# Performance work log

Measured on AMD Instinct MI355X. Metric: run time of the kernel, lower is better.

## Reference

```python
import jax, jax.numpy as jnp
import numpy as np

K_F = 3
NUM = K_F * K_F - 1      # 8 non-reference neighbors
IDX_REF = NUM // 2       # 4
PROP_TIME = 6
PAD = (K_F - 1) // 2


def _bilinear(img, ys, xs):
    """img: [B,H,W]; ys, xs: [B,K,H,W] float sample positions.
    Bilinear interpolation with zero padding (per-corner validity), matching
    mmcv modulated deformable conv sampling."""
    B, H, W = img.shape
    y0 = jnp.floor(ys); x0 = jnp.floor(xs)
    wy = ys - y0; wx = xs - x0
    y0i = y0.astype(jnp.int32); x0i = x0.astype(jnp.int32)
    b = jnp.arange(B).reshape(B, 1, 1, 1)

    def g(yi, xi):
        valid = (yi >= 0) & (yi < H) & (xi >= 0) & (xi < W)
        v = img[b, jnp.clip(yi, 0, H - 1), jnp.clip(xi, 0, W - 1)]
        return jnp.where(valid, v, 0.0)

    return (g(y0i, x0i) * (1 - wy) * (1 - wx)
            + g(y0i, x0i + 1) * (1 - wy) * wx
            + g(y0i + 1, x0i) * wy * (1 - wx)
            + g(y0i + 1, x0i + 1) * wy * wx)


def setup_inputs() -> dict:
    key = jax.random.key(0)
    ks = jax.random.split(key, 6)
    B, Cg, H, W = 4, 64, 240, 1216
    return {
        "feat_init": jax.random.normal(ks[0], (B, 1, H, W), jnp.float32),
        "guidance": jax.random.normal(ks[1], (B, Cg, H, W), jnp.float32),
        "confidence": jax.random.uniform(ks[2], (B, 1, H, W), dtype=jnp.float32),
        "feat_fix": jax.random.normal(ks[3], (B, 1, H, W), jnp.float32),
        "conv_w": jax.random.normal(ks[4], (3 * NUM, Cg, 3, 3), jnp.float32) * 0.05,
        "conv_b": jax.random.normal(ks[5], (3 * NUM,), jnp.float32) * 0.01,
        "aff_scale_const": jnp.full((1,), 0.5 * NUM, jnp.float32),  # affinity_gamma * num (TGASS)
    }


def reference(feat_init, guidance, confidence, feat_fix, conv_w, conv_b, aff_scale_const):
    B, _, H, W = guidance.shape
    dt = guidance.dtype
    sg = jax.lax.stop_gradient

    # offset/affinity head: [B, 3*num, H, W]
    oa = jax.lax.conv_general_dilated(
        guidance, conv_w, (1, 1), ((PAD, PAD), (PAD, PAD)),
        dimension_numbers=("NCHW", "OIHW", "NCHW")) + conv_b[None, :, None, None]
    o1, o2, aff = oa[:, :NUM], oa[:, NUM:2 * NUM], oa[:, 2 * NUM:]

    # insert zero offset at reference position -> [B, 9, H, W] each
    zero = jnp.zeros((B, 1, H, W), dt)
    dy = jnp.concatenate([o1[:, :IDX_REF], zero, o1[:, IDX_REF:]], axis=1)
    dx = jnp.concatenate([o2[:, :IDX_REF], zero, o2[:, IDX_REF:]], axis=1)

    # TGASS affinity
    aff = jnp.tanh(aff) / (aff_scale_const[0] + 1e-8)

    # confidence propagation: 1x1 deform conv (w_conf=1, b=0, pad=0) per
    # non-center kernel point, offsets detached -> bilinear sample of confidence
    idx_nc = jnp.array([0, 1, 2, 3, 5, 6, 7, 8])
    hgrid = jnp.arange(H, dtype=dt)[:, None]
    wgrid = jnp.arange(W, dtype=dt)
    conf_aff = _bilinear(confidence[:, 0],
                         sg(dy[:, idx_nc]) + hgrid,
                         sg(dx[:, idx_nc]) + wgrid)  # [B,8,H,W]
    aff = aff * conf_aff

    # normalize (ASS/TGASS clamp sum to >= 1)
    s = jnp.maximum(jnp.sum(jnp.abs(aff), axis=1, keepdims=True) + 1e-4, 1.0)
    aff = aff / s
    aff_ref = 1.0 - jnp.sum(aff, axis=1, keepdims=True)
    aff9 = jnp.concatenate([aff[:, :IDX_REF], aff_ref, aff[:, IDX_REF:]], axis=1)  # [B,9,H,W]

    # 3x3 deformable sampling grid (pad=1, dilation=1, weight=1, bias=0)
    k = jnp.arange(K_F * K_F)
    base_dy = (k // K_F - PAD).astype(dt)[None, :, None, None]
    base_dx = (k % K_F - PAD).astype(dt)[None, :, None, None]
    ys = hgrid + base_dy + dy  # [B,9,H,W]
    xs = wgrid + base_dx + dx

    mask_fix = sg((feat_fix > 0.0).astype(dt))
    feat = feat_init
    for _ in range(PROP_TIME):
        feat = (1.0 - mask_fix) * feat + mask_fix * feat_fix
        feat = jnp.sum(aff9 * _bilinear(feat[:, 0], ys, xs), axis=1, keepdims=True)

    offset_flat = jnp.stack([dy, dx], axis=2).reshape(B, 2 * (NUM + 1), H, W)
    return feat, offset_flat, aff9
```

## Files before the change

### kernel.cpp

```cpp
#include <hip/hip_runtime.h>
#include <hip/hip_bf16.h>
#include <math.h>

#define B_ 4
#define CG_ 64
#define H_ 240
#define W_ 1216
#define NUMK 576
#define WP (W_ + 2)
#define HP (H_ + 2)
#define WPAD (W_ + 4)
#define HPAD (H_ + 4)
#define PPLANE ((size_t)HPAD * WPAD)

#define TCC 32
#define THR 8
#define SRr 10
#define SCc 34
#define NWT2 (W_ / TCC)
#define NHT2 (H_ / THR)
#define NBLK3 (NWT2 * NHT2 * B_)
#define CBS2 260
#define SMEM_BYTES (SRr * SCc * 128)
#define NCHK (SRr * SCc * 8)

#define R5TC 16
#define R5TH 4
#define R5SC 20
#define R5SR 6
#define R5CPAD 72
#define R5NWT (W_ / R5TC)
#define R5NHT (H_ / R5TH)
#define R5NBLK (R5NWT * R5NHT * B_)
#define R5CBS 68

typedef __attribute__((ext_vector_type(8))) short bf16x8;
typedef __attribute__((ext_vector_type(4))) float f32x4;

__device__ __forceinline__ float bilin_zero(const float* __restrict__ img, float y, float x) {
    float y0f = floorf(y), x0f = floorf(x);
    float wy = y - y0f, wx = x - x0f;
    int y0 = (int)y0f, x0 = (int)x0f;
    int y1 = y0 + 1, x1 = x0 + 1;
    bool yv0 = ((unsigned)y0 < (unsigned)H_);
    bool yv1 = ((unsigned)y1 < (unsigned)H_);
    bool xv0 = ((unsigned)x0 < (unsigned)W_);
    bool xv1 = ((unsigned)x1 < (unsigned)W_);
    float v00 = (yv0 && xv0) ? img[y0 * W_ + x0] : 0.f;
    float v01 = (yv0 && xv1) ? img[y0 * W_ + x1] : 0.f;
    float v10 = (yv1 && xv0) ? img[y1 * W_ + x0] : 0.f;
    float v11 = (yv1 && xv1) ? img[y1 * W_ + x1] : 0.f;
    return v00 * (1.f - wy) * (1.f - wx) + v01 * (1.f - wy) * wx
         + v10 * wy * (1.f - wx) + v11 * wy * wx;
}

__device__ __forceinline__ float bilin_pad(const float* __restrict__ imgp, float y, float x) {
    float yc = fminf(fmaxf(y, -2.0f), (float)H_);
    float xc = fminf(fmaxf(x, -2.0f), (float)W_);
    float y0f = floorf(yc), x0f = floorf(xc);
    float wy = yc - y0f, wx = xc - x0f;
    int iy = (int)y0f + 2, ix = (int)x0f + 2;
    const float* p = imgp + iy * WPAD + ix;
    float v00 = p[0], v01 = p[1], v10 = p[WPAD], v11 = p[WPAD + 1];
    return v00 * (1.f - wy) * (1.f - wx) + v01 * (1.f - wy) * wx
         + v10 * wy * (1.f - wx) + v11 * wy * wx;
}

__device__ __forceinline__ void prep_epilogue(
    const float* a24, int b, int h, int w,
    const float* __restrict__ confidence, const float* __restrict__ feat_init,
    const float* __restrict__ feat_fix, float scale,
    float* __restrict__ out_offset, float* __restrict__ out_aff9,
    float* __restrict__ fb0, unsigned* __restrict__ offb, ushort* __restrict__ affb)
{
    const float* confb = confidence + (size_t)b * H_ * W_;
    float dyv[8], dxv[8], av[8];
    float ssum = 0.f;
    #pragma unroll
    for (int j = 0; j < 8; j++) {
        float dy = a24[j];
        float dx = a24[8 + j];
        float a = tanhf(a24[16 + j]) / scale;
        float conf = bilin_zero(confb, (float)h + dy, (float)w + dx);
        a *= conf;
        dyv[j] = dy; dxv[j] = dx; av[j] = a;
        ssum += fabsf(a);
    }
    float s = fmaxf(ssum + 1e-4f, 1.0f);
    float inv_s = 1.0f / s;
    float suma = 0.f;
    #pragma unroll
    for (int j = 0; j < 8; j++) { av[j] *= inv_s; suma += av[j]; }
    const float aref = 1.0f - suma;

    const int hw = h * W_ + w;
    #pragma unroll
    for (int k = 0; k < 9; k++) {
        float dy = (k == 4) ? 0.f : dyv[(k < 4) ? k : k - 1];
        float dx = (k == 4) ? 0.f : dxv[(k < 4) ? k : k - 1];
        float a  = (k == 4) ? aref : av[(k < 4) ? k : k - 1];
        out_offset[((size_t)(b * 18 + 2 * k) * H_) * W_ + hw] = dy;
        out_offset[((size_t)(b * 18 + 2 * k + 1) * H_) * W_ + hw] = dx;
        out_aff9[((size_t)(b * 9 + k) * H_) * W_ + hw] = a;
        if (offb) {
            __hip_bfloat16 hy = __float2bfloat16(dy);
            __hip_bfloat16 hx = __float2bfloat16(dx);
            __hip_bfloat16 ha = __float2bfloat16(a);
            unsigned uy = *(ushort*)&hy, ux = *(ushort*)&hx;
            offb[((size_t)(b * 9 + k) * H_) * W_ + hw] = uy | (ux << 16);
            affb[((size_t)(b * 9 + k) * H_) * W_ + hw] = *(ushort*)&ha;
        }
    }
    const size_t pix = (size_t)b * H_ * W_ + hw;
    float ff = feat_fix[pix];
    float fi = feat_init[pix];
    float m = (ff > 0.f) ? 1.f : 0.f;
    fb0[pix] = (1.f - m) * fi + m * ff;
}

__global__ __launch_bounds__(256) void zero_pad_kernel(float4* __restrict__ p, int n4) {
    int i = blockIdx.x * 256 + threadIdx.x;
    if (i < n4) p[i] = make_float4(0.f, 0.f, 0.f, 0.f);
}

__global__ __launch_bounds__(256) void pad_conf_kernel(
    const float* __restrict__ confidence, float* __restrict__ confp)
{
    int i = blockIdx.x * 256 + threadIdx.x;
    const int n = B_ * HPAD * WPAD;
    if (i >= n) return;
    int col = i % WPAD;
    int row = (i / WPAD) % HPAD;
    int b = i / (WPAD * HPAD);
    int gh = row - 2, gw = col - 2;
    float v = 0.f;
    if ((unsigned)gh < (unsigned)H_ && (unsigned)gw < (unsigned)W_)
        v = confidence[((size_t)b * H_ + gh) * W_ + gw];
    confp[i] = v;
}

__global__ __launch_bounds__(256) void repack_w_kernel(
    const float* __restrict__ conv_w, __hip_bfloat16* __restrict__ wfrag)
{
    int i = blockIdx.x * 256 + threadIdx.x;
    if (i >= 32 * NUMK) return;
    int e = i & 7;
    int p = (i >> 3) & 15;
    int g = (i >> 7) & 3;
    int half = (i >> 9) & 1;
    int s = i >> 10;
    int m = half * 16 + p;
    int kp = s * 32 + g * 8 + e;
    int tap = kp / 64, c = kp % 64;
    float v = (m < 24) ? conv_w[m * NUMK + c * 9 + tap] : 0.f;
    wfrag[i] = __float2bfloat16(v);
}

__global__ __launch_bounds__(256) void transpose_kernel(
    const float* __restrict__ guidance, __hip_bfloat16* __restrict__ gbf)
{
    __shared__ __align__(16) __hip_bfloat16 tl[64 * 72];
    const int tid = threadIdx.x;
    const int w0 = blockIdx.x * 64;
    const int row = blockIdx.y;
    const int b = blockIdx.z;
    const int gh = row - 1;
    __hip_bfloat16* gbfb = gbf + (size_t)b * HP * WP * 64;

    const int px = tid >> 2;
    const int ch0 = (tid & 3) * 16;
    bf16x8 z8 = {};

    if ((unsigned)gh < (unsigned)H_) {
        const int col = tid & 63;
        const int chb = tid >> 6;
        #pragma unroll
        for (int r = 0; r < 16; r++) {
            int ch = r * 4 + chb;
            float v = guidance[(((size_t)b * CG_ + ch) * H_ + gh) * W_ + w0 + col];
            tl[col * 72 + ch] = __float2bfloat16(v);
        }
        __syncthreads();
        __hip_bfloat16* dst = gbfb + ((size_t)row * WP + 1 + w0 + px) * 64 + ch0;
        *(bf16x8*)dst = *(const bf16x8*)&tl[px * 72 + ch0];
        *(bf16x8*)(dst + 8) = *(const bf16x8*)&tl[px * 72 + ch0 + 8];
    } else {
        __hip_bfloat16* dst = gbfb + ((size_t)row * WP + 1 + w0 + px) * 64 + ch0;
        *(bf16x8*)dst = z8;
        *(bf16x8*)(dst + 8) = z8;
    }
    if (blockIdx.x == 0 && tid < 8)
        *(bf16x8*)(gbfb + ((size_t)row * WP) * 64 + tid * 8) = z8;
    if (blockIdx.x == 18 && tid < 8)
        *(bf16x8*)(gbfb + ((size_t)row * WP + WP - 1) * 64 + tid * 8) = z8;
}

__global__ __launch_bounds__(512, 6) void conv_lds_kernel(
    const __hip_bfloat16* __restrict__ gbf, const __hip_bfloat16* __restrict__ wfrag,
    const float* __restrict__ conv_b, const float* __restrict__ confp,
    const float* __restrict__ feat_init, const float* __restrict__ feat_fix,
    const float* __restrict__ aff_scale,
    float* __restrict__ out_offset, float* __restrict__ out_aff9,
    float* __restrict__ fbp0, unsigned* __restrict__ offb, ushort* __restrict__ affb)
{
    __shared__ __align__(16) char smem[SMEM_BYTES];

    const int tid = threadIdx.x;
    int lin = (blockIdx.x & 7) * (NBLK3 / 8) + (blockIdx.x >> 3);
    const int r0 = lin % NHT2;
    const int rest = lin / NHT2;
    const int wt = rest % NWT2;
    const int b  = rest / NWT2;
    const int h0 = r0 * THR;
    const int w0 = wt * TCC;

    {
        const __hip_bfloat16* gsrc = gbf + (size_t)b * HP * WP * 64;
        auto stage_one = [&](int i) {
            int r = i / (SCc * 8);
            int t = i % (SCc * 8);
            int col = t >> 3;
            int chb = t & 7;
            bf16x8 v = *(const bf16x8*)(gsrc + ((size_t)(h0 + r) * WP + w0 + col) * 64 + chb * 8);
            int dst = (r * SCc + col) * 128 + ((chb * 16) ^ ((col & 7) << 4));
            *(bf16x8*)(smem + dst) = v;
        };
        #pragma unroll
        for (int it = 0; it < 5; it++)
            stage_one(tid + it * 512);
        if (tid < NCHK - 5 * 512)
            stage_one(tid + 5 * 512);
    }
    __syncthreads();

    const int lane = tid & 63;
    const int wid  = tid >> 6;
    const int p    = lane & 15;
    const int g    = lane >> 4;

    f32x4 acc[2][2] = {};

    #pragma unroll
    for (int s = 0; s < 18; s++) {
        const int tap = s >> 1;
        const int ky = tap / 3, kx = tap % 3;
        const int c0b = (s & 1) * 64;
        const __hip_bfloat16* wp = wfrag + (size_t)s * 1024 + g * 128 + p * 8;
        bf16x8 a0 = *(const bf16x8*)(wp);
        bf16x8 a1 = *(const bf16x8*)(wp + 512);
        const int srow = wid + ky;
        #pragma unroll
        for (int nf = 0; nf < 2; nf++) {
            int scol = nf * 16 + p + kx;
            int off = (srow * SCc + scol) * 128 + ((c0b + g * 16) ^ ((scol & 7) << 4));
            bf16x8 bv = *(const bf16x8*)(smem + off);
            acc[0][nf] = __builtin_amdgcn_mfma_f32_16x16x32_bf16(a0, bv, acc[0][nf], 0, 0, 0);
            acc[1][nf] = __builtin_amdgcn_mfma_f32_16x16x32_bf16(a1, bv, acc[1][nf], 0, 0, 0);
        }
    }
    __syncthreads();

    float* cbuf = (float*)smem;
    #pragma unroll
    for (int mt = 0; mt < 2; mt++) {
        int ch = mt * 16 + g * 4;
        if (ch < 24) {
            #pragma unroll
            for (int nf = 0; nf < 2; nf++) {
                int px = wid * 32 + nf * 16 + p;
                #pragma unroll
                for (int r = 0; r < 4; r++)
                    cbuf[(size_t)(ch + r) * CBS2 + px] = acc[mt][nf][r];
            }
        }
    }
    __syncthreads();

    {
        const int pxid = tid >> 1;
        const int sub = tid & 1;
        const int h = h0 + (pxid >> 5);
        const int w = w0 + (pxid & 31);
        const float scale = aff_scale[0] + 1e-8f;
        const float* confb = confp + (size_t)b * PPLANE;

        float dyv[4], dxv[4], av[4];
        float part = 0.f;
        #pragma unroll
        for (int jj = 0; jj < 4; jj++) {
            int j = sub * 4 + jj;
            float dy = cbuf[(size_t)j * CBS2 + pxid] + conv_b[j];
            float dx = cbuf[(size_t)(8 + j) * CBS2 + pxid] + conv_b[8 + j];
            float a = tanhf(cbuf[(size_t)(16 + j) * CBS2 + pxid] + conv_b[16 + j]) / scale;
            float conf = bilin_pad(confb, (float)h + dy, (float)w + dx);
            a *= conf;
            dyv[jj] = dy; dxv[jj] = dx; av[jj] = a;
            part += fabsf(a);
        }
        float ssum = part + __shfl_xor(part, 1);
        float s = fmaxf(ssum + 1e-4f, 1.0f);
        float inv_s = 1.0f / s;
        float sp = 0.f;
        #pragma unroll
        for (int jj = 0; jj < 4; jj++) { av[jj] *= inv_s; sp += av[jj]; }
        float suma = sp + __shfl_xor(sp, 1);

        const int hw = h * W_ + w;
        auto store_k = [&](int k, float dy, float dx, float a) {
            out_offset[((size_t)(b * 18 + 2 * k) * H_) * W_ + hw] = dy;
            out_offset[((size_t)(b * 18 + 2 * k + 1) * H_) * W_ + hw] = dx;
            out_aff9[((size_t)(b * 9 + k) * H_) * W_ + hw] = a;
            __hip_bfloat16 hy = __float2bfloat16(dy);
            __hip_bfloat16 hx = __float2bfloat16(dx);
            __hip_bfloat16 ha = __float2bfloat16(a);
            unsigned uy = *(ushort*)&hy, ux = *(ushort*)&hx;
            offb[((size_t)(b * 9 + k) * H_) * W_ + hw] = uy | (ux << 16);
            affb[((size_t)(b * 9 + k) * H_) * W_ + hw] = *(ushort*)&ha;
        };
        if (sub == 0) {
            #pragma unroll
            for (int jj = 0; jj < 4; jj++)
                store_k(jj, dyv[jj], dxv[jj], av[jj]);
            store_k(4, 0.f, 0.f, 1.0f - suma);
            const size_t pix = (size_t)b * H_ * W_ + hw;
            float ff = feat_fix[pix];
            float fi = feat_init[pix];
            float m = (ff > 0.f) ? 1.f : 0.f;
            fbp0[(size_t)b * PPLANE + (size_t)(h + 2) * WPAD + (w + 2)] =
                (1.f - m) * fi + m * ff;
        } else {
            #pragma unroll
            for (int jj = 0; jj < 4; jj++)
                store_k(5 + jj, dyv[jj], dxv[jj], av[jj]);
        }
    }
}

__global__ __launch_bounds__(256) void prop_packed_kernel(
    const float* __restrict__ fbp_in, const unsigned* __restrict__ offb,
    const ushort* __restrict__ affb, const float* __restrict__ feat_fix,
    float* __restrict__ out, int do_blend, int out_padded)
{
    const int tpx = blockIdx.x * 256 + threadIdx.x;
    const int n2 = (B_ * H_ * W_) / 2;
    if (tpx >= n2) return;
    const int idx = tpx * 2;
    const int w = idx % W_;
    const int h = (idx / W_) % H_;
    const int b = idx / (W_ * H_);
    const float* fbb = fbp_in + (size_t)b * PPLANE;
    const int hw = h * W_ + w;

    float sum0 = 0.f, sum1 = 0.f;
    #pragma unroll
    for (int k = 0; k < 9; k++) {
        const size_t pb = ((size_t)(b * 9 + k) * H_) * W_ + hw;
        uint2 uo = *(const uint2*)(offb + pb);
        unsigned ua = *(const unsigned*)(affb + pb);
        float yb = (float)h + (float)(k / 3 - 1);
        float xb = (float)w + (float)(k % 3 - 1);
        float dy0 = __uint_as_float(uo.x << 16);
        float dx0 = __uint_as_float(uo.x & 0xFFFF0000u);
        float a0  = __uint_as_float(ua << 16);
        sum0 += a0 * bilin_pad(fbb, yb + dy0, xb + dx0);
        float dy1 = __uint_as_float(uo.y << 16);
        float dx1 = __uint_as_float(uo.y & 0xFFFF0000u);
        float a1  = __uint_as_float(ua & 0xFFFF0000u);
        sum1 += a1 * bilin_pad(fbb, yb + dy1, xb + 1.0f + dx1);
    }
    if (do_blend) {
        float2 ff = *(const float2*)(feat_fix + idx);
        if (ff.x > 0.f) sum0 = ff.x;
        if (ff.y > 0.f) sum1 = ff.y;
    }
    if (out_padded) {
        float* o = out + (size_t)b * PPLANE + (size_t)(h + 2) * WPAD + (w + 2);
        *(float2*)o = make_float2(sum0, sum1);
    } else {
        *(float2*)(out + idx) = make_float2(sum0, sum1);
    }
}

__global__ __launch_bounds__(256, 8) void conv_mfma_r5(
    const float* __restrict__ guidance, const __hip_bfloat16* __restrict__ wfrag,
    const float* __restrict__ conv_b, const float* __restrict__ confidence,
    const float* __restrict__ feat_init, const float* __restrict__ feat_fix,
    const float* __restrict__ aff_scale,
    float* __restrict__ out_offset, float* __restrict__ out_aff9,
    float* __restrict__ fb0)
{
    __shared__ __align__(16) __hip_bfloat16 gl[R5SR * R5SC * R5CPAD];
    const int tid = threadIdx.x;
    int lin = (blockIdx.x & 7) * (R5NBLK / 8) + (blockIdx.x >> 3);
    const int r0 = lin % R5NHT;
    const int rest = lin / R5NHT;
    const int wt = rest % R5NWT;
    const int b  = rest / R5NWT;
    const int h0 = r0 * R5TH;
    const int w0 = wt * R5TC;
    {
        auto stage_one = [&](int i) {
            int col = i % R5SC;
            int rest2 = i / R5SC;
            int kr = rest2 % R5SR;
            int c4 = rest2 / R5SR;
            int gh = h0 - 1 + kr;
            int gw = w0 - 2 + col;
            bool vok = ((unsigned)gh < (unsigned)H_) & ((unsigned)gw < (unsigned)W_);
            union { unsigned long long u; __hip_bfloat16 hv[4]; } pk;
            const float* src = guidance + (((size_t)b * CG_ + c4 * 4) * H_ + gh) * W_ + gw;
            #pragma unroll
            for (int j = 0; j < 4; j++) {
                float v = vok ? src[(size_t)j * H_ * W_] : 0.f;
                pk.hv[j] = __float2bfloat16(v);
            }
            *(unsigned long long*)&gl[(size_t)(kr * R5SC + col) * R5CPAD + c4 * 4] = pk.u;
        };
        #pragma unroll
        for (int it = 0; it < 7; it++) stage_one(tid + it * 256);
        if (tid < R5SR * R5SC * 16 - 7 * 256) stage_one(tid + 7 * 256);
    }
    __syncthreads();
    const int lane = tid & 63;
    const int wid  = tid >> 6;
    const int p    = lane & 15;
    const int g    = lane >> 4;
    f32x4 acc[2] = {};
    #pragma unroll
    for (int s = 0; s < 18; s++) {
        const int tap = s >> 1;
        const int ky = tap / 3, kx = tap % 3;
        const int c0 = (s & 1) * 32;
        const __hip_bfloat16* wp = wfrag + (size_t)s * 1024 + g * 128 + p * 8;
        bf16x8 a0 = *(const bf16x8*)(wp);
        bf16x8 a1 = *(const bf16x8*)(wp + 512);
        int cb = p + kx + 1;
        bf16x8 b0 = *(const bf16x8*)(gl + (size_t)((wid + ky) * R5SC + cb) * R5CPAD + c0 + g * 8);
        acc[0] = __builtin_amdgcn_mfma_f32_16x16x32_bf16(a0, b0, acc[0], 0, 0, 0);
        acc[1] = __builtin_amdgcn_mfma_f32_16x16x32_bf16(a1, b0, acc[1], 0, 0, 0);
    }
    __syncthreads();
    float* cbuf = (float*)gl;
    #pragma unroll
    for (int mt = 0; mt < 2; mt++) {
        int ch = mt * 16 + g * 4;
        if (ch < 24) {
            int px = wid * 16 + p;
            #pragma unroll
            for (int r = 0; r < 4; r++)
                cbuf[(size_t)(ch + r) * R5CBS + px] = acc[mt][r];
        }
    }
    __syncthreads();
    if (tid < R5TH * R5TC) {
        const int h = h0 + (tid >> 4);
        const int w = w0 + (tid & 15);
        float a24[24];
        #pragma unroll
        for (int ch = 0; ch < 24; ch++)
            a24[ch] = cbuf[(size_t)ch * R5CBS + tid] + conv_b[ch];
        prep_epilogue(a24, b, h, w, confidence, feat_init, feat_fix,
                      aff_scale[0] + 1e-8f, out_offset, out_aff9, fb0,
                      (unsigned*)nullptr, (ushort*)nullptr);
    }
}

__global__ __launch_bounds__(256) void prop_f32_kernel(
    const float* __restrict__ fb_in, const float* __restrict__ offset,
    const float* __restrict__ aff9, const float* __restrict__ feat_fix,
    float* __restrict__ out, int do_blend)
{
    const int idx = blockIdx.x * 256 + threadIdx.x;
    const int n = B_ * H_ * W_;
    if (idx >= n) return;
    const int w = idx % W_;
    const int h = (idx / W_) % H_;
    const int b = idx / (W_ * H_);
    const float* fbb = fb_in + (size_t)b * H_ * W_;
    const int hw = h * W_ + w;
    float sum = 0.f;
    #pragma unroll
    for (int k = 0; k < 9; k++) {
        float dy = offset[((size_t)(b * 18 + 2 * k) * H_) * W_ + hw];
        float dx = offset[((size_t)(b * 18 + 2 * k + 1) * H_) * W_ + hw];
        float a  = aff9[((size_t)(b * 9 + k) * H_) * W_ + hw];
        float y = (float)h + (float)(k / 3 - 1) + dy;
        float x = (float)w + (float)(k % 3 - 1) + dx;
        sum += a * bilin_zero(fbb, y, x);
    }
    if (do_blend) {
        float ff = feat_fix[idx];
        float m = (ff > 0.f) ? 1.f : 0.f;
        sum = (1.f - m) * sum + m * ff;
    }
    out[idx] = sum;
}

extern "C" void kernel_launch(void* const* d_in, const int* in_sizes, int n_in,
                              void* d_out, int out_size, void* d_ws, size_t ws_size,
                              hipStream_t stream) {
    const float* feat_init  = (const float*)d_in[0];
    const float* guidance   = (const float*)d_in[1];
    const float* confidence = (const float*)d_in[2];
    const float* feat_fix   = (const float*)d_in[3];
    const float* conv_w     = (const float*)d_in[4];
    const float* conv_b     = (const float*)d_in[5];
    const float* aff_scale  = (const float*)d_in[6];

    float* out_feat = (float*)d_out;
    const size_t P1 = (size_t)B_ * H_ * W_;
    float* out_offset = out_feat + P1;
    float* out_aff9   = out_offset + 18 * P1;

    char* ws = (char*)d_ws;
    float* fb0 = (float*)ws;                                   ws += P1 * 4;
    float* fb1 = (float*)ws;                                   ws += P1 * 4;
    __hip_bfloat16* wfrag = (__hip_bfloat16*)ws;               ws += 32 * NUMK * 2;
    unsigned* offb = (unsigned*)ws;                            ws += 9 * P1 * 4;
    ushort* affb = (ushort*)ws;                                ws += 9 * P1 * 2;
    __hip_bfloat16* gbf = (__hip_bfloat16*)ws;                 ws += (size_t)B_ * HP * WP * 64 * 2;
    float* fbp0 = (float*)ws;                                  ws += B_ * PPLANE * 4;
    float* fbp1 = (float*)ws;                                  ws += B_ * PPLANE * 4;
    float* confp = (float*)ws;                                 ws += B_ * PPLANE * 4;
    const size_t need = (size_t)(ws - (char*)d_ws);

    repack_w_kernel<<<(32 * NUMK + 255) / 256, 256, 0, stream>>>(conv_w, wfrag);

    const int n = (int)P1;

    if (ws_size >= need) {
        const int n4 = (int)(2 * B_ * PPLANE / 4);
        zero_pad_kernel<<<(n4 + 255) / 256, 256, 0, stream>>>((float4*)fbp0, n4);
        const int nc = B_ * HPAD * WPAD;
        pad_conf_kernel<<<(nc + 255) / 256, 256, 0, stream>>>(confidence, confp);
        transpose_kernel<<<dim3(19, HP, B_), 256, 0, stream>>>(guidance, gbf);
        conv_lds_kernel<<<NBLK3, 512, 0, stream>>>(
            gbf, wfrag, conv_b, confp, feat_init, feat_fix, aff_scale,
            out_offset, out_aff9, fbp0, offb, affb);
        const int p2blocks = (n / 2 + 255) / 256;
        float* pbufs[2] = {fbp0, fbp1};
        for (int it = 0; it < 6; it++) {
            const float* in = pbufs[it & 1];
            float* o = (it == 5) ? out_feat : pbufs[(it + 1) & 1];
            prop_packed_kernel<<<p2blocks, 256, 0, stream>>>(
                in, offb, affb, feat_fix, o, (it < 5) ? 1 : 0, (it < 5) ? 1 : 0);
        }
    } else {
        const int pblocks = (n + 255) / 256;
        float* bufs[2] = {fb0, fb1};
        conv_mfma_r5<<<R5NBLK, 256, 0, stream>>>(
            guidance, wfrag, conv_b, confidence, feat_init, feat_fix, aff_scale,
            out_offset, out_aff9, fb0);
        for (int it = 0; it < 6; it++) {
            const float* in = bufs[it & 1];
            float* o = (it == 5) ? out_feat : bufs[(it + 1) & 1];
            prop_f32_kernel<<<pblocks, 256, 0, stream>>>(
                in, out_offset, out_aff9, feat_fix, o, (it < 5) ? 1 : 0);
        }
    }
}
```

Baseline: 395.6 us.

## Halve conv tile height and merge zero-pad and confidence-pad kernels

The conv kernel tile shrinks from 8 to 4 output rows per block. Each warp now computes one 16-pixel column fragment instead of two, and four threads share each pixel in the epilogue, with an extra shuffle level for the sums. LDS use drops and launch bounds rise to 8 blocks per SM, aiming at more occupancy and more blocks. The cost is more halo re-staging per output pixel, since 6 staged rows now serve 4 output rows where 10 served 8. The separate zero-fill and confidence-pad kernels are fused into one launch over the three contiguous padded buffers, saving a launch.

```diff
diff --git a/kernel.cpp b/kernel.cpp
--- a/kernel.cpp
+++ b/kernel.cpp
@@ -14,13 +14,13 @@
 #define PPLANE ((size_t)HPAD * WPAD)
 
 #define TCC 32
-#define THR 8
-#define SRr 10
+#define THR 4
+#define SRr 6
 #define SCc 34
 #define NWT2 (W_ / TCC)
 #define NHT2 (H_ / THR)
 #define NBLK3 (NWT2 * NHT2 * B_)
-#define CBS2 260
+#define CBS2 132
 #define SMEM_BYTES (SRr * SCc * 128)
 #define NCHK (SRr * SCc * 8)
 
@@ -118,25 +118,24 @@
     fb0[pix] = (1.f - m) * fi + m * ff;
 }
 
-__global__ __launch_bounds__(256) void zero_pad_kernel(float4* __restrict__ p, int n4) {
+__global__ __launch_bounds__(256) void init_pads_kernel(
+    const float* __restrict__ confidence, float* __restrict__ base)
+{
+    const int n = (int)(3 * B_ * PPLANE);
     int i = blockIdx.x * 256 + threadIdx.x;
-    if (i < n4) p[i] = make_float4(0.f, 0.f, 0.f, 0.f);
-}
-
-__global__ __launch_bounds__(256) void pad_conf_kernel(
-    const float* __restrict__ confidence, float* __restrict__ confp)
-{
-    int i = blockIdx.x * 256 + threadIdx.x;
-    const int n = B_ * HPAD * WPAD;
     if (i >= n) return;
-    int col = i % WPAD;
-    int row = (i / WPAD) % HPAD;
-    int b = i / (WPAD * HPAD);
-    int gh = row - 2, gw = col - 2;
     float v = 0.f;
-    if ((unsigned)gh < (unsigned)H_ && (unsigned)gw < (unsigned)W_)
-        v = confidence[((size_t)b * H_ + gh) * W_ + gw];
-    confp[i] = v;
+    const int cbase = (int)(2 * B_ * PPLANE);
+    if (i >= cbase) {
+        int local = i - cbase;
+        int col = local % WPAD;
+        int row = (local / WPAD) % HPAD;
+        int b = local / (int)PPLANE;
+        int gh = row - 2, gw = col - 2;
+        if ((unsigned)gh < (unsigned)H_ && (unsigned)gw < (unsigned)W_)
+            v = confidence[((size_t)b * H_ + gh) * W_ + gw];
+    }
+    base[i] = v;
 }
 
 __global__ __launch_bounds__(256) void repack_w_kernel(
@@ -195,7 +194,7 @@
         *(bf16x8*)(gbfb + ((size_t)row * WP + WP - 1) * 64 + tid * 8) = z8;
 }
 
-__global__ __launch_bounds__(512, 6) void conv_lds_kernel(
+__global__ __launch_bounds__(512, 8) void conv_lds_kernel(
     const __hip_bfloat16* __restrict__ gbf, const __hip_bfloat16* __restrict__ wfrag,
     const float* __restrict__ conv_b, const float* __restrict__ confp,
     const float* __restrict__ feat_init, const float* __restrict__ feat_fix,
@@ -226,19 +225,21 @@
             *(bf16x8*)(smem + dst) = v;
         };
         #pragma unroll
-        for (int it = 0; it < 5; it++)
+        for (int it = 0; it < 3; it++)
             stage_one(tid + it * 512);
-        if (tid < NCHK - 5 * 512)
-            stage_one(tid + 5 * 512);
+        if (tid < NCHK - 3 * 512)
+            stage_one(tid + 3 * 512);
     }
     __syncthreads();
 
     const int lane = tid & 63;
     const int wid  = tid >> 6;
+    const int wrow = wid >> 1;
+    const int ch16 = (wid & 1) * 16;
     const int p    = lane & 15;
     const int g    = lane >> 4;
 
-    f32x4 acc[2][2] = {};
+    f32x4 acc[2] = {};
 
     #pragma unroll
     for (int s = 0; s < 18; s++) {
@@ -248,15 +249,12 @@
         const __hip_bfloat16* wp = wfrag + (size_t)s * 1024 + g * 128 + p * 8;
         bf16x8 a0 = *(const bf16x8*)(wp);
         bf16x8 a1 = *(const bf16x8*)(wp + 512);
-        const int srow = wid + ky;
-        #pragma unroll
-        for (int nf = 0; nf < 2; nf++) {
-            int scol = nf * 16 + p + kx;
-            int off = (srow * SCc + scol) * 128 + ((c0b + g * 16) ^ ((scol & 7) << 4));
-            bf16x8 bv = *(const bf16x8*)(smem + off);
-            acc[0][nf] = __builtin_amdgcn_mfma_f32_16x16x32_bf16(a0, bv, acc[0][nf], 0, 0, 0);
-            acc[1][nf] = __builtin_amdgcn_mfma_f32_16x16x32_bf16(a1, bv, acc[1][nf], 0, 0, 0);
-        }
+        const int srow = wrow + ky;
+        const int scol = ch16 + p + kx;
+        int off = (srow * SCc + scol) * 128 + ((c0b + g * 16) ^ ((scol & 7) << 4));
+        bf16x8 bv = *(const bf16x8*)(smem + off);
+        acc[0] = __builtin_amdgcn_mfma_f32_16x16x32_bf16(a0, bv, acc[0], 0, 0, 0);
+        acc[1] = __builtin_amdgcn_mfma_f32_16x16x32_bf16(a1, bv, acc[1], 0, 0, 0);
     }
     __syncthreads();
 
@@ -265,30 +263,27 @@
     for (int mt = 0; mt < 2; mt++) {
         int ch = mt * 16 + g * 4;
         if (ch < 24) {
+            int px = wrow * 32 + ch16 + p;
             #pragma unroll
-            for (int nf = 0; nf < 2; nf++) {
-                int px = wid * 32 + nf * 16 + p;
-                #pragma unroll
-                for (int r = 0; r < 4; r++)
-                    cbuf[(size_t)(ch + r) * CBS2 + px] = acc[mt][nf][r];
-            }
+            for (int r = 0; r < 4; r++)
+                cbuf[(size_t)(ch + r) * CBS2 + px] = acc[mt][r];
         }
     }
     __syncthreads();
 
     {
-        const int pxid = tid >> 1;
-        const int sub = tid & 1;
+        const int pxid = tid >> 2;
+        const int sub = tid & 3;
         const int h = h0 + (pxid >> 5);
         const int w = w0 + (pxid & 31);
         const float scale = aff_scale[0] + 1e-8f;
         const float* confb = confp + (size_t)b * PPLANE;
 
-        float dyv[4], dxv[4], av[4];
+        float dyv[2], dxv[2], av[2];
         float part = 0.f;
         #pragma unroll
-        for (int jj = 0; jj < 4; jj++) {
-            int j = sub * 4 + jj;
+        for (int jj = 0; jj < 2; jj++) {
+            int j = sub * 2 + jj;
             float dy = cbuf[(size_t)j * CBS2 + pxid] + conv_b[j];
             float dx = cbuf[(size_t)(8 + j) * CBS2 + pxid] + conv_b[8 + j];
             float a = tanhf(cbuf[(size_t)(16 + j) * CBS2 + pxid] + conv_b[16 + j]) / scale;
@@ -298,12 +293,13 @@
             part += fabsf(a);
         }
         float ssum = part + __shfl_xor(part, 1);
+        ssum += __shfl_xor(ssum, 2);
         float s = fmaxf(ssum + 1e-4f, 1.0f);
         float inv_s = 1.0f / s;
-        float sp = 0.f;
-        #pragma unroll
-        for (int jj = 0; jj < 4; jj++) { av[jj] *= inv_s; sp += av[jj]; }
+        av[0] *= inv_s; av[1] *= inv_s;
+        float sp = av[0] + av[1];
         float suma = sp + __shfl_xor(sp, 1);
+        suma += __shfl_xor(suma, 2);
 
         const int hw = h * W_ + w;
         auto store_k = [&](int k, float dy, float dx, float a) {
@@ -317,10 +313,13 @@
             offb[((size_t)(b * 9 + k) * H_) * W_ + hw] = uy | (ux << 16);
             affb[((size_t)(b * 9 + k) * H_) * W_ + hw] = *(ushort*)&ha;
         };
+        #pragma unroll
+        for (int jj = 0; jj < 2; jj++) {
+            int j = sub * 2 + jj;
+            int k = (j < 4) ? j : j + 1;
+            store_k(k, dyv[jj], dxv[jj], av[jj]);
+        }
         if (sub == 0) {
-            #pragma unroll
-            for (int jj = 0; jj < 4; jj++)
-                store_k(jj, dyv[jj], dxv[jj], av[jj]);
             store_k(4, 0.f, 0.f, 1.0f - suma);
             const size_t pix = (size_t)b * H_ * W_ + hw;
             float ff = feat_fix[pix];
@@ -328,10 +327,6 @@
             float m = (ff > 0.f) ? 1.f : 0.f;
             fbp0[(size_t)b * PPLANE + (size_t)(h + 2) * WPAD + (w + 2)] =
                 (1.f - m) * fi + m * ff;
-        } else {
-            #pragma unroll
-            for (int jj = 0; jj < 4; jj++)
-                store_k(5 + jj, dyv[jj], dxv[jj], av[jj]);
         }
     }
 }
@@ -529,10 +524,8 @@
     const int n = (int)P1;
 
     if (ws_size >= need) {
-        const int n4 = (int)(2 * B_ * PPLANE / 4);
-        zero_pad_kernel<<<(n4 + 255) / 256, 256, 0, stream>>>((float4*)fbp0, n4);
-        const int nc = B_ * HPAD * WPAD;
-        pad_conf_kernel<<<(nc + 255) / 256, 256, 0, stream>>>(confidence, confp);
+        const int ni = (int)(3 * B_ * PPLANE);
+        init_pads_kernel<<<(ni + 255) / 256, 256, 0, stream>>>(confidence, fbp0);
         transpose_kernel<<<dim3(19, HP, B_), 256, 0, stream>>>(guidance, gbf);
         conv_lds_kernel<<<NBLK3, 512, 0, stream>>>(
             gbf, wfrag, conv_b, confp, feat_init, feat_fix, aff_scale,
```

Result: slower. 440.0 us (+11.2%).

## Stage conv weights through LDS in two halves and merge pad-init kernels

Applied to the files above, without the earlier changes.

The conv kernel now copies the repacked bf16 weight fragments into LDS in two 9-step halves, with extra barriers between them, instead of loading them from global memory on every MFMA step. Occupancy bounds drop from 6 to 4 blocks because LDS use per block grows. The separate zero-pad and confidence-pad kernels are merged into a single init kernel that writes all three padded planes. The merged kernel does scalar float writes where the old zero fill used float4 writes, which saves one launch but may cost some write efficiency.

```diff
diff --git a/kernel.cpp b/kernel.cpp
--- a/kernel.cpp
+++ b/kernel.cpp
@@ -21,7 +21,9 @@
 #define NHT2 (H_ / THR)
 #define NBLK3 (NWT2 * NHT2 * B_)
 #define CBS2 260
-#define SMEM_BYTES (SRr * SCc * 128)
+#define SMEM_TILE (SRr * SCc * 128)
+#define WBUF_BYTES (9 * 1024 * 2)
+#define SMEM_BYTES (SMEM_TILE + WBUF_BYTES)
 #define NCHK (SRr * SCc * 8)
 
 #define R5TC 16
@@ -118,25 +120,24 @@
     fb0[pix] = (1.f - m) * fi + m * ff;
 }
 
-__global__ __launch_bounds__(256) void zero_pad_kernel(float4* __restrict__ p, int n4) {
+__global__ __launch_bounds__(256) void init_pads_kernel(
+    const float* __restrict__ confidence, float* __restrict__ base)
+{
+    const int n = (int)(3 * B_ * PPLANE);
     int i = blockIdx.x * 256 + threadIdx.x;
-    if (i < n4) p[i] = make_float4(0.f, 0.f, 0.f, 0.f);
-}
-
-__global__ __launch_bounds__(256) void pad_conf_kernel(
-    const float* __restrict__ confidence, float* __restrict__ confp)
-{
-    int i = blockIdx.x * 256 + threadIdx.x;
-    const int n = B_ * HPAD * WPAD;
     if (i >= n) return;
-    int col = i % WPAD;
-    int row = (i / WPAD) % HPAD;
-    int b = i / (WPAD * HPAD);
-    int gh = row - 2, gw = col - 2;
     float v = 0.f;
-    if ((unsigned)gh < (unsigned)H_ && (unsigned)gw < (unsigned)W_)
-        v = confidence[((size_t)b * H_ + gh) * W_ + gw];
-    confp[i] = v;
+    const int cbase = (int)(2 * B_ * PPLANE);
+    if (i >= cbase) {
+        int local = i - cbase;
+        int col = local % WPAD;
+        int row = (local / WPAD) % HPAD;
+        int b = local / (int)PPLANE;
+        int gh = row - 2, gw = col - 2;
+        if ((unsigned)gh < (unsigned)H_ && (unsigned)gw < (unsigned)W_)
+            v = confidence[((size_t)b * H_ + gh) * W_ + gw];
+    }
+    base[i] = v;
 }
 
 __global__ __launch_bounds__(256) void repack_w_kernel(
@@ -195,7 +196,7 @@
         *(bf16x8*)(gbfb + ((size_t)row * WP + WP - 1) * 64 + tid * 8) = z8;
 }
 
-__global__ __launch_bounds__(512, 6) void conv_lds_kernel(
+__global__ __launch_bounds__(512, 4) void conv_lds_kernel(
     const __hip_bfloat16* __restrict__ gbf, const __hip_bfloat16* __restrict__ wfrag,
     const float* __restrict__ conv_b, const float* __restrict__ confp,
     const float* __restrict__ feat_init, const float* __restrict__ feat_fix,
@@ -204,6 +205,7 @@
     float* __restrict__ fbp0, unsigned* __restrict__ offb, ushort* __restrict__ affb)
 {
     __shared__ __align__(16) char smem[SMEM_BYTES];
+    __hip_bfloat16* wlds = (__hip_bfloat16*)(smem + SMEM_TILE);
 
     const int tid = threadIdx.x;
     int lin = (blockIdx.x & 7) * (NBLK3 / 8) + (blockIdx.x >> 3);
@@ -213,6 +215,19 @@
     const int b  = rest / NWT2;
     const int h0 = r0 * THR;
     const int w0 = wt * TCC;
+
+    auto stage_w = [&](int hf) {
+        const __hip_bfloat16* src = wfrag + hf * 9216;
+        #pragma unroll
+        for (int it = 0; it < 2; it++) {
+            int i = tid + it * 512;
+            *(bf16x8*)(wlds + (size_t)i * 8) = *(const bf16x8*)(src + (size_t)i * 8);
+        }
+        if (tid < 128) {
+            int i = tid + 1024;
+            *(bf16x8*)(wlds + (size_t)i * 8) = *(const bf16x8*)(src + (size_t)i * 8);
+        }
+    };
 
     {
         const __hip_bfloat16* gsrc = gbf + (size_t)b * HP * WP * 64;
@@ -231,6 +246,7 @@
         if (tid < NCHK - 5 * 512)
             stage_one(tid + 5 * 512);
     }
+    stage_w(0);
     __syncthreads();
 
     const int lane = tid & 63;
@@ -241,21 +257,30 @@
     f32x4 acc[2][2] = {};
 
     #pragma unroll
-    for (int s = 0; s < 18; s++) {
-        const int tap = s >> 1;
-        const int ky = tap / 3, kx = tap % 3;
-        const int c0b = (s & 1) * 64;
-        const __hip_bfloat16* wp = wfrag + (size_t)s * 1024 + g * 128 + p * 8;
-        bf16x8 a0 = *(const bf16x8*)(wp);
-        bf16x8 a1 = *(const bf16x8*)(wp + 512);
-        const int srow = wid + ky;
-        #pragma unroll
-        for (int nf = 0; nf < 2; nf++) {
-            int scol = nf * 16 + p + kx;
-            int off = (srow * SCc + scol) * 128 + ((c0b + g * 16) ^ ((scol & 7) << 4));
-            bf16x8 bv = *(const bf16x8*)(smem + off);
-            acc[0][nf] = __builtin_amdgcn_mfma_f32_16x16x32_bf16(a0, bv, acc[0][nf], 0, 0, 0);
-            acc[1][nf] = __builtin_amdgcn_mfma_f32_16x16x32_bf16(a1, bv, acc[1][nf], 0, 0, 0);
+    for (int hf = 0; hf < 2; hf++) {
+        if (hf == 1) {
+            __syncthreads();
+            stage_w(1);
+            __syncthreads();
+        }
+        #pragma unroll
+        for (int sl = 0; sl < 9; sl++) {
+            const int s = hf * 9 + sl;
+            const int tap = s >> 1;
+            const int ky = tap / 3, kx = tap % 3;
+            const int c0b = (s & 1) * 64;
+            const __hip_bfloat16* wp = wlds + (size_t)sl * 1024 + g * 128 + p * 8;
+            bf16x8 a0 = *(const bf16x8*)(wp);
+            bf16x8 a1 = *(const bf16x8*)(wp + 512);
+            const int srow = wid + ky;
+            #pragma unroll
+            for (int nf = 0; nf < 2; nf++) {
+                int scol = nf * 16 + p + kx;
+                int off = (srow * SCc + scol) * 128 + ((c0b + g * 16) ^ ((scol & 7) << 4));
+                bf16x8 bv = *(const bf16x8*)(smem + off);
+                acc[0][nf] = __builtin_amdgcn_mfma_f32_16x16x32_bf16(a0, bv, acc[0][nf], 0, 0, 0);
+                acc[1][nf] = __builtin_amdgcn_mfma_f32_16x16x32_bf16(a1, bv, acc[1][nf], 0, 0, 0);
+            }
         }
     }
     __syncthreads();
@@ -529,10 +554,8 @@
     const int n = (int)P1;
 
     if (ws_size >= need) {
-        const int n4 = (int)(2 * B_ * PPLANE / 4);
-        zero_pad_kernel<<<(n4 + 255) / 256, 256, 0, stream>>>((float4*)fbp0, n4);
-        const int nc = B_ * HPAD * WPAD;
-        pad_conf_kernel<<<(nc + 255) / 256, 256, 0, stream>>>(confidence, confp);
+        const int ni = (int)(3 * B_ * PPLANE);
+        init_pads_kernel<<<(ni + 255) / 256, 256, 0, stream>>>(confidence, fbp0);
         transpose_kernel<<<dim3(19, HP, B_), 256, 0, stream>>>(guidance, gbf);
         conv_lds_kernel<<<NBLK3, 512, 0, stream>>>(
             gbf, wfrag, conv_b, confp, feat_init, feat_fix, aff_scale,
```

After: 383.2 us. -3.1%, faster.
